# Performance work log

Measured on AMD Instinct MI355X. Metric: run time of the kernel, lower is better.

The kernel has to match this reference:

```python
import jax, jax.numpy as jnp
import numpy as np

N = 100000
E = 1600000
IN, HID, OUT = 128, 128, 64


def gcn_conv(x, W, b, src, dst, n):
    # GCNConv with normalize=True and implicit self-loops:
    # out = D^-1/2 (A+I) D^-1/2 (x W) + b
    ew = jnp.ones(src.shape[0], dtype=x.dtype)  # unit edge weights
    deg = jax.ops.segment_sum(ew, dst, num_segments=n)  # in-degree incl. self-loop
    dinv = jnp.where(deg > 0, jax.lax.rsqrt(deg), 0.0)
    norm = dinv[src] * dinv[dst]  # [E+N]
    h = x @ W  # dense transform first (PyG order)
    msg = h[src] * norm[:, None]  # gather + scale (memory-bound)
    return jax.ops.segment_sum(msg, dst, num_segments=n) + b


def setup_inputs() -> dict:
    key = jax.random.key(0)
    k1, k2, k3, k4, k5, k6 = jax.random.split(key, 6)
    x = jax.random.normal(k1, (N, IN), dtype=jnp.float32)
    edge_index = jax.random.randint(k2, (2, E), 0, N, dtype=jnp.int32)
    s1 = 1.0 / np.sqrt(IN)
    s2 = 1.0 / np.sqrt(HID)
    W1 = jax.random.uniform(k3, (IN, HID), jnp.float32, -s1, s1)
    b1 = jax.random.uniform(k4, (HID,), jnp.float32, -s1, s1)
    W2 = jax.random.uniform(k5, (HID, OUT), jnp.float32, -s2, s2)
    b2 = jax.random.uniform(k6, (OUT,), jnp.float32, -s2, s2)
    return {"x": x, "edge_index": edge_index, "W1": W1, "b1": b1, "W2": W2, "b2": b2}


def reference(x, edge_index, W1, b1, W2, b2):
    n = x.shape[0]
    loops = jnp.arange(n, dtype=edge_index.dtype)
    src = jnp.concatenate([edge_index[0], loops])  # add self-loops
    dst = jnp.concatenate([edge_index[1], loops])
    # eval mode: dropout(p=0.5) is identity
    h = jax.nn.relu(gcn_conv(x, W1, b1, src, dst, n))
    out = gcn_conv(h, W2, b2, src, dst, n)
    return out
```

## Files before the change

kernel.cpp:

```cpp
#include <hip/hip_runtime.h>
#include <hip/hip_fp16.h>
#include <type_traits>

#define NBK 256
#define BSHIFT 9
#define NPB 512
#define BCAP 10240
#define CCAP 12288
#define EPB 4096

template <int N> struct alignas(4 * N) HVec { __half2 v[N]; };

typedef _Float16 half8 __attribute__((ext_vector_type(8)));
typedef float f32x4 __attribute__((ext_vector_type(4)));

__global__ void prep0_k(const float* __restrict__ W1, const float* __restrict__ W2,
                        _Float16* __restrict__ WT1, _Float16* __restrict__ WT2,
                        int* __restrict__ cursor) {
    int i = blockIdx.x * blockDim.x + threadIdx.x;
    if (i < NBK) cursor[i] = 0;
    if (i < 128 * 128) {
        int k = i >> 7, j = i & 127;
        WT1[j * 128 + k] = (_Float16)W1[i];
    }
    int i2 = i - 128 * 128;
    if (i2 >= 0 && i2 < 128 * 64) {
        int k = i2 >> 6, j = i2 & 63;
        WT2[j * 128 + k] = (_Float16)W2[i2];
    }
}

__global__ __launch_bounds__(512) void partA_k(const int* __restrict__ src,
                                               const int* __restrict__ dst,
                                               int* __restrict__ cursor,
                                               int* __restrict__ bucketed, int ne) {
    __shared__ int hist[NBK], gbs[NBK];
    int t = threadIdx.x;
    int e0 = blockIdx.x * EPB;
    int e1 = min(e0 + EPB, ne);
    for (int i = t; i < NBK; i += 512) hist[i] = 0;
    __syncthreads();
    int sv[EPB / 512], dv[EPB / 512], rv[EPB / 512];
#pragma unroll
    for (int k = 0; k < EPB / 512; k++) {
        int e = e0 + t + k * 512;
        int s = 0, d = -1, r = 0;
        if (e < e1) {
            s = src[e];
            d = dst[e];
            r = atomicAdd(&hist[d >> BSHIFT], 1);
        }
        sv[k] = s; dv[k] = d; rv[k] = r;
    }
    __syncthreads();
    for (int i = t; i < NBK; i += 512)
        gbs[i] = hist[i] ? atomicAdd(&cursor[i], hist[i]) : 0;
    __syncthreads();
#pragma unroll
    for (int k = 0; k < EPB / 512; k++) {
        if (dv[k] >= 0) {
            int b = dv[k] >> BSHIFT;
            int q = gbs[b] + rv[k];
            if (q < BCAP)
                bucketed[(size_t)b * BCAP + q] = ((dv[k] & (NPB - 1)) << 17) | sv[k];
        }
    }
}

__global__ __launch_bounds__(1024) void csrB_k(const int* __restrict__ bucketed,
                                               const int* __restrict__ cursor,
                                               int* __restrict__ csr,
                                               int* __restrict__ rowbeg,
                                               int* __restrict__ rend,
                                               float* __restrict__ dinv, int nn) {
    __shared__ int cnt[NPB], ofs[NPB], exs[NPB];
    int t = threadIdx.x;
    int b = blockIdx.x;
    int m = min(cursor[b], BCAP);
    const int* bk = bucketed + (size_t)b * BCAP;
    int cbase = b * CCAP;
    if (t < NPB) cnt[t] = 0;
    __syncthreads();
    int rk[(BCAP + 1023) / 1024];
    int nit = 0;
    for (int i = t; i < m; i += 1024)
        rk[nit++] = atomicAdd(&cnt[bk[i] >> 17], 1);
    __syncthreads();
    int v = 0, pv = 0;
    if (t < NPB) { v = cnt[t]; pv = (v + 7) & ~7; ofs[t] = pv; }
    __syncthreads();
    for (int d = 1; d < NPB; d <<= 1) {
        int u = 0;
        if (t < NPB && t >= d) u = ofs[t - d];
        __syncthreads();
        if (t < NPB) ofs[t] += u;
        __syncthreads();
    }
    if (t < NPB) {
        int ex = ofs[t] - pv;
        exs[t] = ex;
        int node = b * NPB + t;
        if (node < nn) {
            rowbeg[node] = cbase + ex;
            rend[node]   = cbase + ex + pv;
            dinv[node] = rsqrtf((float)(v + 1));
        }
    }
    __syncthreads();
    nit = 0;
    for (int i = t; i < m; i += 1024) {
        int e = bk[i];
        csr[cbase + exs[e >> 17] + rk[nit++]] = e & 0x1FFFF;
    }
    if (t < NPB) {
        int ex = exs[t];
        for (int k = v; k < pv; k++) csr[cbase + ex + k] = nn;
    }
}

template <int NO, bool SCALE, typename XT>
__global__ __launch_bounds__(256) void gemm_mfma_k(const XT* __restrict__ X,
                                                   const _Float16* __restrict__ WT,
                                                   const float* __restrict__ dinv,
                                                   _Float16* __restrict__ H, int nrows) {
    constexpr int K = 128;
    constexpr int NCT = NO / 16;
    if (blockIdx.x == 0 && threadIdx.x < NO)
        H[(size_t)nrows * NO + threadIdx.x] = (_Float16)0.f;
    int wv = (int)((blockIdx.x * (size_t)blockDim.x + threadIdx.x) >> 6);
    int r0 = wv * 16;
    if (r0 >= nrows) return;
    int lane = threadIdx.x & 63;
    int lr = lane & 15;
    int kg = lane >> 4;
    int rg = r0 + lr;
    if (rg >= nrows) rg = nrows - 1;

    half8 a[4];
    if constexpr (std::is_same<XT, float>::value) {
#pragma unroll
        for (int ks = 0; ks < 4; ks++) {
            const float* px = X + (size_t)rg * K + ks * 32 + kg * 8;
            float4 x0 = *(const float4*)px;
            float4 x1 = *(const float4*)(px + 4);
            half8 vv;
            vv[0] = (_Float16)x0.x; vv[1] = (_Float16)x0.y;
            vv[2] = (_Float16)x0.z; vv[3] = (_Float16)x0.w;
            vv[4] = (_Float16)x1.x; vv[5] = (_Float16)x1.y;
            vv[6] = (_Float16)x1.z; vv[7] = (_Float16)x1.w;
            a[ks] = vv;
        }
    } else {
#pragma unroll
        for (int ks = 0; ks < 4; ks++)
            a[ks] = *(const half8*)(X + (size_t)rg * K + ks * 32 + kg * 8);
    }

    f32x4 acc[NCT];
#pragma unroll
    for (int ct = 0; ct < NCT; ct++) acc[ct] = (f32x4){0.f, 0.f, 0.f, 0.f};
#pragma unroll
    for (int ct = 0; ct < NCT; ct++) {
#pragma unroll
        for (int ks = 0; ks < 4; ks++) {
            half8 b = *(const half8*)(WT + (size_t)(ct * 16 + lr) * K + ks * 32 + kg * 8);
            acc[ct] = __builtin_amdgcn_mfma_f32_16x16x32_f16(a[ks], b, acc[ct], 0, 0, 0);
        }
    }
#pragma unroll
    for (int i = 0; i < 4; i++) {
        int rr = r0 + kg * 4 + i;
        if (rr < nrows) {
            float s = SCALE ? dinv[rr] : 1.f;
            _Float16* hp = H + (size_t)rr * NO + lr;
#pragma unroll
            for (int ct = 0; ct < NCT; ct++)
                hp[ct * 16] = (_Float16)(acc[ct][i] * s);
        }
    }
}

template <bool RELU, bool OUTSCALE>
__global__ __launch_bounds__(256) void agg128_k(const __half* __restrict__ H,
                                                const int* __restrict__ rowbeg,
                                                const int* __restrict__ rend,
                                                const int* __restrict__ csr,
                                                const float* __restrict__ dinv,
                                                const float* __restrict__ bias,
                                                __half* __restrict__ Out, int nn) {
    constexpr int NF = 128;
    int wid = (int)((blockIdx.x * (size_t)blockDim.x + threadIdx.x) >> 6);
    if (wid >= nn) return;
    int lane = threadIdx.x & 63;
    int g = lane >> 4, t = lane & 15;
    float acc[8];
#pragma unroll
    for (int j = 0; j < 8; j++) acc[j] = 0.f;

    int beg = rowbeg[wid], end = rend[wid];
    int e0 = beg;
    for (; e0 + 16 <= end; e0 += 16) {
        int eb = e0 + g * 4;
        int s0 = csr[eb + 0], s1 = csr[eb + 1], s2 = csr[eb + 2], s3 = csr[eb + 3];
        HVec<4> va = *((const HVec<4>*)(H + (size_t)s0 * NF) + t);
        HVec<4> vb = *((const HVec<4>*)(H + (size_t)s1 * NF) + t);
        HVec<4> vc = *((const HVec<4>*)(H + (size_t)s2 * NF) + t);
        HVec<4> vd = *((const HVec<4>*)(H + (size_t)s3 * NF) + t);
#pragma unroll
        for (int q = 0; q < 4; q++) {
            __half2 pab = __hadd2(va.v[q], vb.v[q]);
            __half2 pcd = __hadd2(vc.v[q], vd.v[q]);
            float2 fab = __half22float2(pab);
            float2 fcd = __half22float2(pcd);
            acc[2 * q + 0] += fab.x + fcd.x;
            acc[2 * q + 1] += fab.y + fcd.y;
        }
    }
    for (; e0 < end; e0 += 4) {
        int s = csr[e0 + g];
        HVec<4> va = *((const HVec<4>*)(H + (size_t)s * NF) + t);
#pragma unroll
        for (int q = 0; q < 4; q++) {
            float2 f = __half22float2(va.v[q]);
            acc[2 * q + 0] += f.x;
            acc[2 * q + 1] += f.y;
        }
    }
#pragma unroll
    for (int j = 0; j < 8; j++) {
        acc[j] += __shfl_xor(acc[j], 16);
        acc[j] += __shfl_xor(acc[j], 32);
    }
    HVec<4> hn = *((const HVec<4>*)(H + (size_t)wid * NF) + t);
#pragma unroll
    for (int q = 0; q < 4; q++) {
        float2 f = __half22float2(hn.v[q]);
        acc[2 * q + 0] += f.x;
        acc[2 * q + 1] += f.y;
    }
    if (g == 0) {
        float dn = dinv[wid];
        float r[8];
#pragma unroll
        for (int j = 0; j < 8; j++) {
            r[j] = acc[j] * dn + bias[t * 8 + j];
            if (RELU) r[j] = fmaxf(r[j], 0.f);
            if (OUTSCALE) r[j] *= dn;
        }
        HVec<4> o;
#pragma unroll
        for (int q = 0; q < 4; q++)
            o.v[q] = __floats2half2_rn(r[2 * q], r[2 * q + 1]);
        *((HVec<4>*)(Out + (size_t)wid * NF) + t) = o;
    }
}

template <bool RELU>
__global__ __launch_bounds__(256) void agg64_k(const __half* __restrict__ H,
                                               const int* __restrict__ rowbeg,
                                               const int* __restrict__ rend,
                                               const int* __restrict__ csr,
                                               const float* __restrict__ dinv,
                                               const float* __restrict__ bias,
                                               float* __restrict__ Out, int nn) {
    constexpr int NF = 64;
    int wid = (int)((blockIdx.x * (size_t)blockDim.x + threadIdx.x) >> 6);
    if (wid >= nn) return;
    int lane = threadIdx.x & 63;
    int g = lane >> 3, t = lane & 7;
    float acc[8];
#pragma unroll
    for (int j = 0; j < 8; j++) acc[j] = 0.f;

    int beg = rowbeg[wid], end = rend[wid];
    int e0 = beg;
    for (; e0 + 16 <= end; e0 += 16) {
        int eb = e0 + g * 2;
        int s0 = csr[eb], s1 = csr[eb + 1];
        HVec<4> va = *((const HVec<4>*)(H + (size_t)s0 * NF) + t);
        HVec<4> vb = *((const HVec<4>*)(H + (size_t)s1 * NF) + t);
#pragma unroll
        for (int q = 0; q < 4; q++) {
            __half2 p = __hadd2(va.v[q], vb.v[q]);
            float2 f = __half22float2(p);
            acc[2 * q + 0] += f.x;
            acc[2 * q + 1] += f.y;
        }
    }
    for (; e0 < end; e0 += 8) {
        int s = csr[e0 + g];
        HVec<4> va = *((const HVec<4>*)(H + (size_t)s * NF) + t);
#pragma unroll
        for (int q = 0; q < 4; q++) {
            float2 f = __half22float2(va.v[q]);
            acc[2 * q + 0] += f.x;
            acc[2 * q + 1] += f.y;
        }
    }
#pragma unroll
    for (int j = 0; j < 8; j++) {
        acc[j] += __shfl_xor(acc[j], 8);
        acc[j] += __shfl_xor(acc[j], 16);
        acc[j] += __shfl_xor(acc[j], 32);
    }
    HVec<4> hn = *((const HVec<4>*)(H + (size_t)wid * NF) + t);
#pragma unroll
    for (int q = 0; q < 4; q++) {
        float2 f = __half22float2(hn.v[q]);
        acc[2 * q + 0] += f.x;
        acc[2 * q + 1] += f.y;
    }
    if (g == 0) {
        float dn = dinv[wid];
        float r[8];
#pragma unroll
        for (int j = 0; j < 8; j++) {
            r[j] = acc[j] * dn + bias[t * 8 + j];
            if (RELU) r[j] = fmaxf(r[j], 0.f);
        }
        float* op = Out + (size_t)wid * NF + t * 8;
        float4 o0, o1;
        o0.x = r[0]; o0.y = r[1]; o0.z = r[2]; o0.w = r[3];
        o1.x = r[4]; o1.y = r[5]; o1.z = r[6]; o1.w = r[7];
        *(float4*)op = o0;
        *(float4*)(op + 4) = o1;
    }
}


extern "C" void kernel_launch(void* const* d_in, const int* in_sizes, int n_in,
                              void* d_out, int out_size, void* d_ws, size_t ws_size,
                              hipStream_t stream) {
    const float* x  = (const float*)d_in[0];
    const int* ei   = (const int*)d_in[1];
    const float* W1 = (const float*)d_in[2];
    const float* b1 = (const float*)d_in[3];
    const float* W2 = (const float*)d_in[4];
    const float* b2 = (const float*)d_in[5];
    float* out = (float*)d_out;

    const int IN = 128, HID = 128;
    int nn = in_sizes[0] / IN;
    int ne = in_sizes[1] / 2;
    const int* src = ei;
    const int* dst = ei + ne;
    int nbuckets = (nn + NPB - 1) / NPB;

    char* w = (char*)d_ws;
    size_t off = 0;
    auto take = [&](size_t bytes) -> void* {
        void* p = w + off;
        off = (off + bytes + 255) & ~(size_t)255;
        return p;
    };
    int*      cursor = (int*)take(NBK * 4);
    int*      rowbeg = (int*)take((size_t)nn * 4);
    int*      rend   = (int*)take((size_t)nn * 4);
    float*    dinv   = (float*)take((size_t)nn * 4);
    int*      csr    = (int*)take((size_t)NBK * CCAP * 4);
    _Float16* WT1    = (_Float16*)take(128 * 128 * 2);
    _Float16* WT2    = (_Float16*)take(64 * 128 * 2);
    _Float16* h      = (_Float16*)take((size_t)(nn + 1) * HID * 2);
    __half*   h1     = (__half*)take((size_t)nn * HID * 2);
    _Float16* h2     = h;
    int*      bucketed = (int*)h;

    (void)ws_size; (void)n_in; (void)out_size;

    int tb = 256;
    prep0_k<<<(128 * 128 + 128 * 64 + tb - 1) / tb, tb, 0, stream>>>(W1, W2, WT1, WT2, cursor);
    partA_k<<<(ne + EPB - 1) / EPB, 512, 0, stream>>>(src, dst, cursor, bucketed, ne);
    csrB_k<<<nbuckets, 1024, 0, stream>>>(bucketed, cursor, csr, rowbeg, rend, dinv, nn);

    int gblocks = ((nn + 15) / 16 + 3) / 4;

    gemm_mfma_k<128, true, float><<<gblocks, tb, 0, stream>>>(x, WT1, dinv, h, nn);
    agg128_k<true, true><<<(nn * 64 + tb - 1) / tb, tb, 0, stream>>>(
        (const __half*)h, rowbeg, rend, csr, dinv, b1, (__half*)h1, nn);

    gemm_mfma_k<64, false, __half><<<gblocks, tb, 0, stream>>>(h1, WT2, dinv, h2, nn);
    agg64_k<false><<<(nn * 64 + tb - 1) / tb, tb, 0, stream>>>(
        (const __half*)h2, rowbeg, rend, csr, dinv, b2, out, nn);
}
```

Baseline: 202.1 us.

## Fuse layer-1 aggregation with layer-2 MFMA GEMM through shared memory

Merges the 128-feature aggregation kernel with the second dense transform. Each 1024-thread block aggregates 16 nodes, one wave per node, stages the ReLU'd and scaled fp16 rows in LDS, and then four waves run the 16x64 MFMA product. This removes the h1 round-trip through global memory and one kernel launch. The cost is a block-wide barrier that makes waves with light rows wait for the heaviest row, idles 12 of 16 waves during the GEMM, and a large block size may lower occupancy flexibility. h2 now gets its own buffer, with a zero padding row written by block 0.

```diff
diff --git a/kernel.cpp b/kernel.cpp
--- a/kernel.cpp
+++ b/kernel.cpp
@@ -180,78 +180,104 @@
     }
 }
 
-template <bool RELU, bool OUTSCALE>
-__global__ __launch_bounds__(256) void agg128_k(const __half* __restrict__ H,
-                                                const int* __restrict__ rowbeg,
-                                                const int* __restrict__ rend,
-                                                const int* __restrict__ csr,
-                                                const float* __restrict__ dinv,
-                                                const float* __restrict__ bias,
-                                                __half* __restrict__ Out, int nn) {
+__global__ __launch_bounds__(1024) void fusedA1G2_k(const __half* __restrict__ H,
+                                                    const int* __restrict__ rowbeg,
+                                                    const int* __restrict__ rend,
+                                                    const int* __restrict__ csr,
+                                                    const float* __restrict__ dinv,
+                                                    const float* __restrict__ b1,
+                                                    const _Float16* __restrict__ WT2,
+                                                    _Float16* __restrict__ H2, int nn) {
     constexpr int NF = 128;
-    int wid = (int)((blockIdx.x * (size_t)blockDim.x + threadIdx.x) >> 6);
-    if (wid >= nn) return;
-    int lane = threadIdx.x & 63;
+    __shared__ _Float16 sh[16][136];
+    int tid = threadIdx.x;
+    int w = tid >> 6;
+    int lane = tid & 63;
     int g = lane >> 4, t = lane & 15;
-    float acc[8];
-#pragma unroll
-    for (int j = 0; j < 8; j++) acc[j] = 0.f;
-
-    int beg = rowbeg[wid], end = rend[wid];
-    int e0 = beg;
-    for (; e0 + 16 <= end; e0 += 16) {
-        int eb = e0 + g * 4;
-        int s0 = csr[eb + 0], s1 = csr[eb + 1], s2 = csr[eb + 2], s3 = csr[eb + 3];
-        HVec<4> va = *((const HVec<4>*)(H + (size_t)s0 * NF) + t);
-        HVec<4> vb = *((const HVec<4>*)(H + (size_t)s1 * NF) + t);
-        HVec<4> vc = *((const HVec<4>*)(H + (size_t)s2 * NF) + t);
-        HVec<4> vd = *((const HVec<4>*)(H + (size_t)s3 * NF) + t);
+    int nid = (int)blockIdx.x * 16 + w;
+    if (blockIdx.x == 0 && tid < 64)
+        H2[(size_t)nn * 64 + tid] = (_Float16)0.f;
+
+    if (nid < nn) {
+        float acc[8];
+#pragma unroll
+        for (int j = 0; j < 8; j++) acc[j] = 0.f;
+        int beg = rowbeg[nid], end = rend[nid];
+        int e0 = beg;
+        for (; e0 + 16 <= end; e0 += 16) {
+            int eb = e0 + g * 4;
+            int s0 = csr[eb + 0], s1 = csr[eb + 1], s2 = csr[eb + 2], s3 = csr[eb + 3];
+            HVec<4> va = *((const HVec<4>*)(H + (size_t)s0 * NF) + t);
+            HVec<4> vb = *((const HVec<4>*)(H + (size_t)s1 * NF) + t);
+            HVec<4> vc = *((const HVec<4>*)(H + (size_t)s2 * NF) + t);
+            HVec<4> vd = *((const HVec<4>*)(H + (size_t)s3 * NF) + t);
+#pragma unroll
+            for (int q = 0; q < 4; q++) {
+                __half2 pab = __hadd2(va.v[q], vb.v[q]);
+                __half2 pcd = __hadd2(vc.v[q], vd.v[q]);
+                float2 fab = __half22float2(pab);
+                float2 fcd = __half22float2(pcd);
+                acc[2 * q + 0] += fab.x + fcd.x;
+                acc[2 * q + 1] += fab.y + fcd.y;
+            }
+        }
+        for (; e0 < end; e0 += 4) {
+            int s = csr[e0 + g];
+            HVec<4> va = *((const HVec<4>*)(H + (size_t)s * NF) + t);
+#pragma unroll
+            for (int q = 0; q < 4; q++) {
+                float2 f = __half22float2(va.v[q]);
+                acc[2 * q + 0] += f.x;
+                acc[2 * q + 1] += f.y;
+            }
+        }
+#pragma unroll
+        for (int j = 0; j < 8; j++) {
+            acc[j] += __shfl_xor(acc[j], 16);
+            acc[j] += __shfl_xor(acc[j], 32);
+        }
+        HVec<4> hn = *((const HVec<4>*)(H + (size_t)nid * NF) + t);
 #pragma unroll
         for (int q = 0; q < 4; q++) {
-            __half2 pab = __hadd2(va.v[q], vb.v[q]);
-            __half2 pcd = __hadd2(vc.v[q], vd.v[q]);
-            float2 fab = __half22float2(pab);
-            float2 fcd = __half22float2(pcd);
-            acc[2 * q + 0] += fab.x + fcd.x;
-            acc[2 * q + 1] += fab.y + fcd.y;
-        }
-    }
-    for (; e0 < end; e0 += 4) {
-        int s = csr[e0 + g];
-        HVec<4> va = *((const HVec<4>*)(H + (size_t)s * NF) + t);
-#pragma unroll
-        for (int q = 0; q < 4; q++) {
-            float2 f = __half22float2(va.v[q]);
+            float2 f = __half22float2(hn.v[q]);
             acc[2 * q + 0] += f.x;
             acc[2 * q + 1] += f.y;
         }
-    }
-#pragma unroll
-    for (int j = 0; j < 8; j++) {
-        acc[j] += __shfl_xor(acc[j], 16);
-        acc[j] += __shfl_xor(acc[j], 32);
-    }
-    HVec<4> hn = *((const HVec<4>*)(H + (size_t)wid * NF) + t);
-#pragma unroll
-    for (int q = 0; q < 4; q++) {
-        float2 f = __half22float2(hn.v[q]);
-        acc[2 * q + 0] += f.x;
-        acc[2 * q + 1] += f.y;
-    }
-    if (g == 0) {
-        float dn = dinv[wid];
-        float r[8];
-#pragma unroll
-        for (int j = 0; j < 8; j++) {
-            r[j] = acc[j] * dn + bias[t * 8 + j];
-            if (RELU) r[j] = fmaxf(r[j], 0.f);
-            if (OUTSCALE) r[j] *= dn;
-        }
-        HVec<4> o;
-#pragma unroll
-        for (int q = 0; q < 4; q++)
-            o.v[q] = __floats2half2_rn(r[2 * q], r[2 * q + 1]);
-        *((HVec<4>*)(Out + (size_t)wid * NF) + t) = o;
+        if (g == 0) {
+            float dn = dinv[nid];
+            float r[8];
+#pragma unroll
+            for (int j = 0; j < 8; j++) {
+                r[j] = acc[j] * dn + b1[t * 8 + j];
+                r[j] = fmaxf(r[j], 0.f);
+                r[j] *= dn;
+            }
+            HVec<4> o;
+#pragma unroll
+            for (int q = 0; q < 4; q++)
+                o.v[q] = __floats2half2_rn(r[2 * q], r[2 * q + 1]);
+            *(HVec<4>*)&sh[w][t * 8] = o;
+        }
+    }
+    __syncthreads();
+    if (w < 4) {
+        int lr = lane & 15, kg = lane >> 4;
+        half8 a[4];
+#pragma unroll
+        for (int ks = 0; ks < 4; ks++)
+            a[ks] = *(const half8*)&sh[lr][ks * 32 + kg * 8];
+        f32x4 acc2 = (f32x4){0.f, 0.f, 0.f, 0.f};
+#pragma unroll
+        for (int ks = 0; ks < 4; ks++) {
+            half8 b = *(const half8*)(WT2 + (size_t)(w * 16 + lr) * 128 + ks * 32 + kg * 8);
+            acc2 = __builtin_amdgcn_mfma_f32_16x16x32_f16(a[ks], b, acc2, 0, 0, 0);
+        }
+#pragma unroll
+        for (int i = 0; i < 4; i++) {
+            int rr = (int)blockIdx.x * 16 + kg * 4 + i;
+            if (rr < nn)
+                H2[(size_t)rr * 64 + w * 16 + lr] = (_Float16)acc2[i];
+        }
     }
 }
 
@@ -361,8 +387,7 @@
     _Float16* WT1    = (_Float16*)take(128 * 128 * 2);
     _Float16* WT2    = (_Float16*)take(64 * 128 * 2);
     _Float16* h      = (_Float16*)take((size_t)(nn + 1) * HID * 2);
-    __half*   h1     = (__half*)take((size_t)nn * HID * 2);
-    _Float16* h2     = h;
+    _Float16* h2     = (_Float16*)take((size_t)(nn + 1) * 64 * 2);
     int*      bucketed = (int*)h;
 
     (void)ws_size; (void)n_in; (void)out_size;
@@ -375,10 +400,8 @@
     int gblocks = ((nn + 15) / 16 + 3) / 4;
 
     gemm_mfma_k<128, true, float><<<gblocks, tb, 0, stream>>>(x, WT1, dinv, h, nn);
-    agg128_k<true, true><<<(nn * 64 + tb - 1) / tb, tb, 0, stream>>>(
-        (const __half*)h, rowbeg, rend, csr, dinv, b1, (__half*)h1, nn);
-
-    gemm_mfma_k<64, false, __half><<<gblocks, tb, 0, stream>>>(h1, WT2, dinv, h2, nn);
+    fusedA1G2_k<<<(nn + 15) / 16, 1024, 0, stream>>>(
+        (const __half*)h, rowbeg, rend, csr, dinv, b1, WT2, h2, nn);
     agg64_k<false><<<(nn * 64 + tb - 1) / tb, tb, 0, stream>>>(
         (const __half*)h2, rowbeg, rend, csr, dinv, b2, out, nn);
 }
```

Measured after the change: 197.2 us. 2.4% less time.
